# Kernel tuning notes

Hardware: AMD Instinct MI355X
Metric: run time of the kernel (lower is better)

The kernel has to match this reference:

```python
import jax, jax.numpy as jnp
import numpy as np

N_NODES = 100000
N_EDGES = 1600000
EMB = 64
H1 = 128
H2 = 64


def gcn_conv(x, edge_index, W, b, num_nodes):
    # PyG GCNConv: x' = D^{-1/2}(A+I)D^{-1/2} (x W) + b, with self-loops
    x = x @ W  # [N, out]
    src, dst = edge_index[0], edge_index[1]
    loop = jnp.arange(num_nodes, dtype=src.dtype)
    src_f = jnp.concatenate([src, loop])
    dst_f = jnp.concatenate([dst, loop])
    deg = jax.ops.segment_sum(jnp.ones_like(src_f, dtype=x.dtype), dst_f,
                              num_segments=num_nodes)
    dinv = jnp.where(deg > 0, jax.lax.rsqrt(deg), 0.0)
    norm = dinv[src_f] * dinv[dst_f]           # [E+N]
    msg = x[src_f] * norm[:, None]             # gather + scale
    out = jax.ops.segment_sum(msg, dst_f, num_segments=num_nodes)
    return out + b


def setup_inputs() -> dict:
    key = jax.random.key(0)
    ks = jax.random.split(key, 12)
    category_ids = jax.random.randint(ks[0], (N_NODES,), 0, 1000)
    sub_category_ids = jax.random.randint(ks[1], (N_NODES,), 0, 5000)
    element_ids = jax.random.randint(ks[2], (N_NODES,), 0, 100000)
    edge_index = jax.random.randint(ks[3], (2, N_EDGES), 0, N_NODES)
    cat_table = jax.random.normal(ks[4], (1000, EMB), dtype=jnp.float32)
    sub_table = jax.random.normal(ks[5], (5000, EMB), dtype=jnp.float32)
    elem_table = jax.random.normal(ks[6], (100000, EMB), dtype=jnp.float32)
    W1 = jax.random.normal(ks[7], (3 * EMB, H1), dtype=jnp.float32) * (1.0 / np.sqrt(3 * EMB))
    b1 = jnp.zeros((H1,), dtype=jnp.float32)
    W2 = jax.random.normal(ks[8], (H1, H2), dtype=jnp.float32) * (1.0 / np.sqrt(H1))
    b2 = jnp.zeros((H2,), dtype=jnp.float32)
    return {
        "category_ids": category_ids,
        "sub_category_ids": sub_category_ids,
        "element_ids": element_ids,
        "edge_index": edge_index,
        "cat_table": cat_table,
        "sub_table": sub_table,
        "elem_table": elem_table,
        "W1": W1, "b1": b1, "W2": W2, "b2": b2,
    }


def reference(category_ids, sub_category_ids, element_ids, edge_index,
              cat_table, sub_table, elem_table, W1, b1, W2, b2):
    # NodeEmbedding: concat of three 64-dim lookups -> [N, 192]
    x = jnp.concatenate([cat_table[category_ids],
                         sub_table[sub_category_ids],
                         elem_table[element_ids]], axis=-1)
    x = jax.nn.relu(gcn_conv(x, edge_index, W1, b1, N_NODES))
    # dropout(0.3) is identity in eval mode
    x = jax.nn.relu(gcn_conv(x, edge_index, W2, b2, N_NODES))
    return x
```

## Files before the change

### kernel.cpp

```cpp
#include <hip/hip_runtime.h>

#define N_NODES 100000
#define EMB     64
#define H1      128
#define H2      64

#define BSHIFT  7
#define NBUCK   782
#define CAP     3072

#define OFF_DINV  0
#define OFF_ROWP  100004
#define OFF_COL   200008
#define OFF_GFILL 1800008
#define OFF_GBASE 1800792
#define OFF_SCR   1801576
#define OFF_H     4203880
#define OFF_Y     10603880
#define OFF_PCAT  17003880
#define OFF_PSUB  17131880

static __device__ __forceinline__ unsigned short f2bf(float f) {
    unsigned int u = __float_as_uint(f);
    unsigned int r = (u + 0x7fffu + ((u >> 16) & 1u)) >> 16;
    return (unsigned short)r;
}
static __device__ __forceinline__ unsigned int pack2bf(float a, float b) {
    return (unsigned int)f2bf(a) | ((unsigned int)f2bf(b) << 16);
}
static __device__ __forceinline__ float bflo(unsigned int u) {
    return __uint_as_float(u << 16);
}
static __device__ __forceinline__ float bfhi(unsigned int u) {
    return __uint_as_float(u & 0xffff0000u);
}


__global__ __launch_bounds__(1024) void k_bin(
    const int* __restrict__ src, const int* __restrict__ dst, int E,
    int* __restrict__ gfill, unsigned int* __restrict__ scr)
{
    __shared__ int hist[NBUCK];
    __shared__ int basec[NBUCK];
    int t = threadIdx.x;
    for (int i = t; i < NBUCK; i += 1024) hist[i] = 0;
    __syncthreads();
    int chunk = (E + gridDim.x - 1) / gridDim.x;
    int e0 = blockIdx.x * chunk;
    int e1 = min(e0 + chunk, E);
    for (int i = e0 + t; i < e1; i += 1024)
        atomicAdd(&hist[dst[i] >> BSHIFT], 1);
    __syncthreads();
    for (int b = t; b < NBUCK; b += 1024) {
        int c = hist[b];
        basec[b] = (c > 0) ? atomicAdd(&gfill[b], c) : 0;
        hist[b] = 0;
    }
    __syncthreads();
    for (int i = e0 + t; i < e1; i += 1024) {
        int d = dst[i];
        int b = d >> BSHIFT;
        int slot = basec[b] + atomicAdd(&hist[b], 1);
        if (slot < CAP)
            scr[(size_t)b * CAP + slot] =
                ((unsigned int)(d & 127) << 17) | (unsigned int)src[i];
    }
}


__global__ __launch_bounds__(256) void k_bscan(
    const int* __restrict__ gfill, int* __restrict__ gbase,
    int* __restrict__ rowp, int E)
{
    __shared__ int sh[256];
    int t = threadIdx.x;
    int v[4]; int s = 0;
    #pragma unroll
    for (int u = 0; u < 4; ++u) {
        int i = t * 4 + u;
        v[u] = (i < NBUCK) ? gfill[i] : 0;
        s += v[u];
    }
    sh[t] = s;
    __syncthreads();
    for (int off = 1; off < 256; off <<= 1) {
        int x = (t >= off) ? sh[t - off] : 0;
        __syncthreads();
        sh[t] += x;
        __syncthreads();
    }
    int run = (t == 0) ? 0 : sh[t - 1];
    #pragma unroll
    for (int u = 0; u < 4; ++u) {
        int i = t * 4 + u;
        if (i < NBUCK) gbase[i] = run;
        run += v[u];
    }
    if (t == 255) { gbase[NBUCK] = run; rowp[N_NODES] = E; }
}


__global__ __launch_bounds__(512) void k_csr(
    const unsigned int* __restrict__ scr, const int* __restrict__ gfill,
    const int* __restrict__ gbase, int N,
    int* __restrict__ rowp, int* __restrict__ col, float* __restrict__ dinv)
{
    __shared__ unsigned int stage[CAP];
    __shared__ int hist[128];
    __shared__ int offs[128];
    __shared__ int cur[128];
    int b = blockIdx.x, t = threadIdx.x;
    int cnt = gfill[b];
    if (cnt > CAP) cnt = CAP;
    int base = gbase[b];
    if (t < 128) hist[t] = 0;
    __syncthreads();
    for (int i = t; i < cnt; i += 512) {
        unsigned int p = scr[(size_t)b * CAP + i];
        stage[i] = p;
        atomicAdd(&hist[p >> 17], 1);
    }
    __syncthreads();
    if (t < 128) offs[t] = hist[t];
    __syncthreads();
    for (int off = 1; off < 128; off <<= 1) {
        int x = 0;
        if (t < 128 && t >= off) x = offs[t - off];
        __syncthreads();
        if (t < 128) offs[t] += x;
        __syncthreads();
    }
    if (t < 128) {
        int excl = offs[t] - hist[t];
        cur[t] = 0;
        int d = b * 128 + t;
        if (d < N) {
            rowp[d] = base + excl;
            dinv[d] = rsqrtf((float)(hist[t] + 1));
        }
        offs[t] = excl;
    }
    __syncthreads();
    for (int i = t; i < cnt; i += 512) {
        unsigned int p = stage[i];
        int dl = (int)(p >> 17);
        int pos = offs[dl] + atomicAdd(&cur[dl], 1);
        col[base + pos] = (int)(p & 0x1FFFFu);
    }
}


__global__ __launch_bounds__(256) void k_ptab(
    const float* __restrict__ tab, const float* __restrict__ Wseg,
    float* __restrict__ P, int R)
{
    __shared__ float Wl[64][128];
    int t = threadIdx.x;
    for (int idx = t; idx < 64 * 128; idx += 256)
        Wl[idx >> 7][idx & 127] = Wseg[idx];
    __syncthreads();
    int cg = t & 31, ng = t >> 5;
    int r = blockIdx.x * 8 + ng;
    if (r >= R) return;
    const float* x = tab + (size_t)r * 64;
    float4 acc = make_float4(0.f, 0.f, 0.f, 0.f);
    #pragma unroll 8
    for (int k = 0; k < 64; ++k) {
        float xx = x[k];
        float4 w = *(const float4*)&Wl[k][cg * 4];
        acc.x += xx * w.x; acc.y += xx * w.y;
        acc.z += xx * w.z; acc.w += xx * w.w;
    }
    *(float4*)&P[(size_t)r * 128 + cg * 4] = acc;
}


__global__ __launch_bounds__(256) void k_gemm1(
    const int* __restrict__ cid, const int* __restrict__ sid, const int* __restrict__ eid,
    const float* __restrict__ elem_t, const float* __restrict__ W1,
    const float* __restrict__ Pcat, const float* __restrict__ Psub,
    const float* __restrict__ dinv,
    unsigned short* __restrict__ hb, int N)
{
    __shared__ float Wl[64][128];
    int t = threadIdx.x;
    const float* Wc = W1 + 128 * 128;
    for (int idx = t; idx < 64 * 128; idx += 256)
        Wl[idx >> 7][idx & 127] = Wc[idx];
    __syncthreads();

    int cg = t & 31;
    int ng = t >> 5;
    int n0 = blockIdx.x << 6;

    const float* rp[8];
    #pragma unroll
    for (int i = 0; i < 8; ++i) {
        int n = n0 + ng + 8 * i;
        int id = eid[(n < N) ? n : 0];
        rp[i] = elem_t + (size_t)id * 64;
    }
    float4 acc[8];
    #pragma unroll
    for (int i = 0; i < 8; ++i) acc[i] = make_float4(0.f, 0.f, 0.f, 0.f);

    #pragma unroll 4
    for (int k4 = 0; k4 < 16; ++k4) {
        float4 xv[8];
        #pragma unroll
        for (int i = 0; i < 8; ++i)
            xv[i] = *(const float4*)(rp[i] + k4 * 4);
        #pragma unroll
        for (int kk = 0; kk < 4; ++kk) {
            float4 w = *(const float4*)&Wl[k4 * 4 + kk][cg * 4];
            #pragma unroll
            for (int i = 0; i < 8; ++i) {
                float xx = (kk == 0) ? xv[i].x : (kk == 1) ? xv[i].y
                         : (kk == 2) ? xv[i].z : xv[i].w;
                acc[i].x += xx * w.x;
                acc[i].y += xx * w.y;
                acc[i].z += xx * w.z;
                acc[i].w += xx * w.w;
            }
        }
    }
    #pragma unroll
    for (int i = 0; i < 8; ++i) {
        int n = n0 + ng + 8 * i;
        if (n < N) {
            float4 pc = *(const float4*)&Pcat[(size_t)cid[n] * 128 + cg * 4];
            float4 ps = *(const float4*)&Psub[(size_t)sid[n] * 128 + cg * 4];
            float s = dinv[n];
            uint2 p;
            p.x = pack2bf((acc[i].x + pc.x + ps.x) * s, (acc[i].y + pc.y + ps.y) * s);
            p.y = pack2bf((acc[i].z + pc.z + ps.z) * s, (acc[i].w + pc.w + ps.w) * s);
            *(uint2*)(hb + (size_t)n * 128 + cg * 4) = p;
        }
    }
}


__global__ __launch_bounds__(256) void k_gemm2(
    const unsigned int* __restrict__ yb, const float* __restrict__ W2,
    const float* __restrict__ dinv,
    unsigned short* __restrict__ h2b, int N)
{
    __shared__ float Wl[128][64];
    int t = threadIdx.x;
    for (int idx = t; idx < 128 * 64; idx += 256)
        Wl[idx >> 6][idx & 63] = W2[idx];
    __syncthreads();

    int cg = t & 15;
    int ng = t >> 4;
    int n0 = blockIdx.x << 7;
    const unsigned int* rp[8];
    float4 acc[8];
    #pragma unroll
    for (int i = 0; i < 8; ++i) {
        acc[i] = make_float4(0.f, 0.f, 0.f, 0.f);
        int n = n0 + ng + 16 * i;
        rp[i] = yb + (size_t)((n < N) ? n : (N - 1)) * 64;
    }
    #pragma unroll 4
    for (int k4 = 0; k4 < 32; ++k4) {
        uint2 xv[8];
        #pragma unroll
        for (int i = 0; i < 8; ++i)
            xv[i] = *(const uint2*)(rp[i] + k4 * 2);
        #pragma unroll
        for (int kk = 0; kk < 4; ++kk) {
            float4 w = *(const float4*)&Wl[k4 * 4 + kk][cg * 4];
            #pragma unroll
            for (int i = 0; i < 8; ++i) {
                float xx = (kk == 0) ? bflo(xv[i].x) : (kk == 1) ? bfhi(xv[i].x)
                         : (kk == 2) ? bflo(xv[i].y) : bfhi(xv[i].y);
                acc[i].x += xx * w.x;
                acc[i].y += xx * w.y;
                acc[i].z += xx * w.z;
                acc[i].w += xx * w.w;
            }
        }
    }
    #pragma unroll
    for (int i = 0; i < 8; ++i) {
        int n = n0 + ng + 16 * i;
        if (n < N) {
            float s = dinv[n];
            uint2 p;
            p.x = pack2bf(acc[i].x * s, acc[i].y * s);
            p.y = pack2bf(acc[i].z * s, acc[i].w * s);
            *(uint2*)(h2b + (size_t)n * 64 + cg * 4) = p;
        }
    }
}


__global__ __launch_bounds__(256) void k_agg1(
    const unsigned short* __restrict__ hb, const int* __restrict__ rowp,
    const int* __restrict__ col, const float* __restrict__ dinv,
    const float* __restrict__ b1, unsigned int* __restrict__ yb, int N)
{
    int wv = threadIdx.x >> 6;
    int lane = threadIdx.x & 63;
    int d = blockIdx.x * 4 + wv;
    if (d >= N) return;
    const unsigned int* hp = (const unsigned int*)hb;
    float dd = dinv[d];
    unsigned int su = hp[(size_t)d * 64 + lane];
    float ax0 = bflo(su), ay0 = bfhi(su);
    float ax1 = 0.f, ay1 = 0.f, ax2 = 0.f, ay2 = 0.f, ax3 = 0.f, ay3 = 0.f;
    float ax4 = 0.f, ay4 = 0.f, ax5 = 0.f, ay5 = 0.f, ax6 = 0.f, ay6 = 0.f;
    float ax7 = 0.f, ay7 = 0.f;
    int e0 = rowp[d];
    int len = rowp[d + 1] - e0;
    for (int i = 0; i < len; i += 8) {
        int c[8];
        #pragma unroll
        for (int k = 0; k < 8; ++k)
            c[k] = col[(i + k) < len ? (e0 + i + k) : e0];
        #pragma unroll
        for (int k = 0; k < 8; ++k) {
            bool pr = (i + k) < len;
            int idx = pr ? c[k] : d;
            float m = pr ? 1.f : 0.f;
            unsigned int u = hp[(size_t)idx * 64 + lane];
            float vx = m * bflo(u), vy = m * bfhi(u);
            switch (k) {
                case 0: ax0 += vx; ay0 += vy; break;
                case 1: ax1 += vx; ay1 += vy; break;
                case 2: ax2 += vx; ay2 += vy; break;
                case 3: ax3 += vx; ay3 += vy; break;
                case 4: ax4 += vx; ay4 += vy; break;
                case 5: ax5 += vx; ay5 += vy; break;
                case 6: ax6 += vx; ay6 += vy; break;
                default: ax7 += vx; ay7 += vy; break;
            }
        }
    }
    float2 bb = *(const float2*)&b1[lane * 2];
    float rx = dd * (((ax0 + ax1) + (ax2 + ax3)) + ((ax4 + ax5) + (ax6 + ax7))) + bb.x;
    float ry = dd * (((ay0 + ay1) + (ay2 + ay3)) + ((ay4 + ay5) + (ay6 + ay7))) + bb.y;
    yb[(size_t)d * 64 + lane] = pack2bf(rx > 0.f ? rx : 0.f, ry > 0.f ? ry : 0.f);
}


__global__ __launch_bounds__(256) void k_agg2(
    const unsigned short* __restrict__ h2b, const int* __restrict__ rowp,
    const int* __restrict__ col, const float* __restrict__ dinv,
    const float* __restrict__ b2, float* __restrict__ out, int N)
{
    int wv = threadIdx.x >> 6;
    int lane = threadIdx.x & 63;
    int d = blockIdx.x * 4 + wv;
    if (d >= N) return;
    float dd = dinv[d];
    float a0 = __uint_as_float((unsigned int)h2b[(size_t)d * 64 + lane] << 16);
    float a1 = 0.f, a2 = 0.f, a3 = 0.f, a4 = 0.f, a5 = 0.f, a6 = 0.f, a7 = 0.f;
    int e0 = rowp[d];
    int len = rowp[d + 1] - e0;
    for (int i = 0; i < len; i += 8) {
        int c[8];
        #pragma unroll
        for (int k = 0; k < 8; ++k)
            c[k] = col[(i + k) < len ? (e0 + i + k) : e0];
        #pragma unroll
        for (int k = 0; k < 8; ++k) {
            bool pr = (i + k) < len;
            int idx = pr ? c[k] : d;
            float m = pr ? 1.f : 0.f;
            float v = m * __uint_as_float((unsigned int)h2b[(size_t)idx * 64 + lane] << 16);
            switch (k) {
                case 0: a0 += v; break;
                case 1: a1 += v; break;
                case 2: a2 += v; break;
                case 3: a3 += v; break;
                case 4: a4 += v; break;
                case 5: a5 += v; break;
                case 6: a6 += v; break;
                default: a7 += v; break;
            }
        }
    }
    float v = dd * (((a0 + a1) + (a2 + a3)) + ((a4 + a5) + (a6 + a7))) + b2[lane];
    out[(size_t)d * 64 + lane] = v > 0.f ? v : 0.f;
}


extern "C" void kernel_launch(void* const* d_in, const int* in_sizes, int n_in,
                              void* d_out, int out_size, void* d_ws, size_t ws_size,
                              hipStream_t stream) {
    const int*   cid    = (const int*)d_in[0];
    const int*   sid    = (const int*)d_in[1];
    const int*   eid    = (const int*)d_in[2];
    const int*   edge   = (const int*)d_in[3];
    const float* cat_t  = (const float*)d_in[4];
    const float* sub_t  = (const float*)d_in[5];
    const float* elem_t = (const float*)d_in[6];
    const float* W1     = (const float*)d_in[7];
    const float* b1     = (const float*)d_in[8];
    const float* W2     = (const float*)d_in[9];
    const float* b2     = (const float*)d_in[10];
    float* out = (float*)d_out;

    int N = in_sizes[0];
    int E = in_sizes[3] / 2;
    const int* src = edge;
    const int* dst = edge + E;

    int*   ws    = (int*)d_ws;
    float* dinv  = (float*)(ws + OFF_DINV);
    int*   rowp  = ws + OFF_ROWP;
    int*   col   = ws + OFF_COL;
    int*   gfill = ws + OFF_GFILL;
    int*   gbase = ws + OFF_GBASE;
    unsigned int* scr = (unsigned int*)(ws + OFF_SCR);
    unsigned short* hb = (unsigned short*)(ws + OFF_H);
    unsigned int*   yb = (unsigned int*)(ws + OFF_Y);
    float* Pcat = (float*)(ws + OFF_PCAT);
    float* Psub = (float*)(ws + OFF_PSUB);

    hipMemsetAsync(gfill, 0, NBUCK * sizeof(int), stream);

    k_ptab<<<125, 256, 0, stream>>>(cat_t, W1,            Pcat, 1000);
    k_ptab<<<625, 256, 0, stream>>>(sub_t, W1 + 64 * 128, Psub, 5000);

    k_bin<<<200, 1024, 0, stream>>>(src, dst, E, gfill, scr);
    k_bscan<<<1, 256, 0, stream>>>(gfill, gbase, rowp, E);
    k_csr<<<NBUCK, 512, 0, stream>>>(scr, gfill, gbase, N, rowp, col, dinv);

    k_gemm1<<<(N + 63) / 64, 256, 0, stream>>>(cid, sid, eid, elem_t, W1, Pcat, Psub, dinv, hb, N);
    k_agg1<<<(N + 3) / 4, 256, 0, stream>>>(hb, rowp, col, dinv, b1, yb, N);
    k_gemm2<<<(N + 127) / 128, 256, 0, stream>>>(yb, W2, dinv, hb, N);
    k_agg2<<<(N + 3) / 4, 256, 0, stream>>>(hb, rowp, col, dinv, b2, out, N);
}
```

Baseline: 391.0 us.

## Process two destination nodes per wavefront with wider vector gathers in aggregation

Both aggregation kernels now assign two destination nodes to each 64-lane wavefront, one per 32-lane half. Each lane gathers wider vectors: uint2 (4 bf16) in agg1, and in agg2 a 32-bit pair of bf16 instead of a single 16-bit value. The aim is fewer, wider memory transactions per neighbour row and half as many wavefronts. The trade-off is divergence: both halves loop to the larger of the two degrees, with masked loads for the shorter row.

Result: no change. 386.3 us (-1.2%).

```diff
diff --git a/kernel.cpp b/kernel.cpp
--- a/kernel.cpp
+++ b/kernel.cpp
@@ -301,47 +301,55 @@
     const int* __restrict__ col, const float* __restrict__ dinv,
     const float* __restrict__ b1, unsigned int* __restrict__ yb, int N)
 {
-    int wv = threadIdx.x >> 6;
+    int w = blockIdx.x * 4 + (threadIdx.x >> 6);
     int lane = threadIdx.x & 63;
-    int d = blockIdx.x * 4 + wv;
-    if (d >= N) return;
+    int half = lane >> 5, l5 = lane & 31;
+    int d0 = w * 2;
+    if (d0 >= N) return;
+    int d = d0 + half;
+    if (d >= N) d = N - 1;
     const unsigned int* hp = (const unsigned int*)hb;
     float dd = dinv[d];
-    unsigned int su = hp[(size_t)d * 64 + lane];
-    float ax0 = bflo(su), ay0 = bfhi(su);
-    float ax1 = 0.f, ay1 = 0.f, ax2 = 0.f, ay2 = 0.f, ax3 = 0.f, ay3 = 0.f;
-    float ax4 = 0.f, ay4 = 0.f, ax5 = 0.f, ay5 = 0.f, ax6 = 0.f, ay6 = 0.f;
-    float ax7 = 0.f, ay7 = 0.f;
-    int e0 = rowp[d];
-    int len = rowp[d + 1] - e0;
-    for (int i = 0; i < len; i += 8) {
-        int c[8];
-        #pragma unroll
-        for (int k = 0; k < 8; ++k)
-            c[k] = col[(i + k) < len ? (e0 + i + k) : e0];
-        #pragma unroll
-        for (int k = 0; k < 8; ++k) {
+    unsigned base = ((unsigned)d << 6) + (l5 << 1);
+    uint2 su = *(const uint2*)(hp + base);
+    float s00 = bflo(su.x), s01 = bfhi(su.x), s02 = bflo(su.y), s03 = bfhi(su.y);
+    float s10 = 0.f, s11 = 0.f, s12 = 0.f, s13 = 0.f;
+    float s20 = 0.f, s21 = 0.f, s22 = 0.f, s23 = 0.f;
+    float s30 = 0.f, s31 = 0.f, s32 = 0.f, s33 = 0.f;
+    int eb = rowp[d];
+    int len = rowp[d + 1] - eb;
+    int lo = __shfl_xor(len, 32);
+    int lm = len > lo ? len : lo;
+    for (int i = 0; i < lm; i += 4) {
+        int cc[4];
+        #pragma unroll
+        for (int k = 0; k < 4; ++k)
+            cc[k] = col[(i + k) < len ? (eb + i + k) : 0];
+        #pragma unroll
+        for (int k = 0; k < 4; ++k) {
             bool pr = (i + k) < len;
-            int idx = pr ? c[k] : d;
+            int idx = pr ? cc[k] : d;
             float m = pr ? 1.f : 0.f;
-            unsigned int u = hp[(size_t)idx * 64 + lane];
-            float vx = m * bflo(u), vy = m * bfhi(u);
+            uint2 u = *(const uint2*)(hp + (((unsigned)idx) << 6) + (l5 << 1));
+            float vx = m * bflo(u.x), vy = m * bfhi(u.x);
+            float vz = m * bflo(u.y), vw = m * bfhi(u.y);
             switch (k) {
-                case 0: ax0 += vx; ay0 += vy; break;
-                case 1: ax1 += vx; ay1 += vy; break;
-                case 2: ax2 += vx; ay2 += vy; break;
-                case 3: ax3 += vx; ay3 += vy; break;
-                case 4: ax4 += vx; ay4 += vy; break;
-                case 5: ax5 += vx; ay5 += vy; break;
-                case 6: ax6 += vx; ay6 += vy; break;
-                default: ax7 += vx; ay7 += vy; break;
+                case 0: s00 += vx; s01 += vy; s02 += vz; s03 += vw; break;
+                case 1: s10 += vx; s11 += vy; s12 += vz; s13 += vw; break;
+                case 2: s20 += vx; s21 += vy; s22 += vz; s23 += vw; break;
+                default: s30 += vx; s31 += vy; s32 += vz; s33 += vw; break;
             }
         }
     }
-    float2 bb = *(const float2*)&b1[lane * 2];
-    float rx = dd * (((ax0 + ax1) + (ax2 + ax3)) + ((ax4 + ax5) + (ax6 + ax7))) + bb.x;
-    float ry = dd * (((ay0 + ay1) + (ay2 + ay3)) + ((ay4 + ay5) + (ay6 + ay7))) + bb.y;
-    yb[(size_t)d * 64 + lane] = pack2bf(rx > 0.f ? rx : 0.f, ry > 0.f ? ry : 0.f);
+    float4 bb = *(const float4*)&b1[l5 * 4];
+    float r0 = dd * ((s00 + s10) + (s20 + s30)) + bb.x;
+    float r1 = dd * ((s01 + s11) + (s21 + s31)) + bb.y;
+    float r2 = dd * ((s02 + s12) + (s22 + s32)) + bb.z;
+    float r3 = dd * ((s03 + s13) + (s23 + s33)) + bb.w;
+    uint2 p;
+    p.x = pack2bf(r0 > 0.f ? r0 : 0.f, r1 > 0.f ? r1 : 0.f);
+    p.y = pack2bf(r2 > 0.f ? r2 : 0.f, r3 > 0.f ? r3 : 0.f);
+    *(uint2*)(yb + base) = p;
 }
 
 
@@ -350,40 +358,56 @@
     const int* __restrict__ col, const float* __restrict__ dinv,
     const float* __restrict__ b2, float* __restrict__ out, int N)
 {
-    int wv = threadIdx.x >> 6;
+    int w = blockIdx.x * 4 + (threadIdx.x >> 6);
     int lane = threadIdx.x & 63;
-    int d = blockIdx.x * 4 + wv;
-    if (d >= N) return;
+    int half = lane >> 5, l5 = lane & 31;
+    int d0 = w * 2;
+    if (d0 >= N) return;
+    int d = d0 + half;
+    if (d >= N) d = N - 1;
+    const unsigned int* hp = (const unsigned int*)h2b;
     float dd = dinv[d];
-    float a0 = __uint_as_float((unsigned int)h2b[(size_t)d * 64 + lane] << 16);
-    float a1 = 0.f, a2 = 0.f, a3 = 0.f, a4 = 0.f, a5 = 0.f, a6 = 0.f, a7 = 0.f;
-    int e0 = rowp[d];
-    int len = rowp[d + 1] - e0;
-    for (int i = 0; i < len; i += 8) {
-        int c[8];
+    unsigned base = ((unsigned)d << 5) + l5;
+    unsigned su = hp[base];
+    float s00 = bflo(su), s01 = bfhi(su);
+    float s10 = 0.f, s11 = 0.f, s20 = 0.f, s21 = 0.f, s30 = 0.f, s31 = 0.f;
+    float s40 = 0.f, s41 = 0.f, s50 = 0.f, s51 = 0.f, s60 = 0.f, s61 = 0.f;
+    float s70 = 0.f, s71 = 0.f;
+    int eb = rowp[d];
+    int len = rowp[d + 1] - eb;
+    int lo = __shfl_xor(len, 32);
+    int lm = len > lo ? len : lo;
+    for (int i = 0; i < lm; i += 8) {
+        int cc[8];
         #pragma unroll
         for (int k = 0; k < 8; ++k)
-            c[k] = col[(i + k) < len ? (e0 + i + k) : e0];
+            cc[k] = col[(i + k) < len ? (eb + i + k) : 0];
         #pragma unroll
         for (int k = 0; k < 8; ++k) {
             bool pr = (i + k) < len;
-            int idx = pr ? c[k] : d;
+            int idx = pr ? cc[k] : d;
             float m = pr ? 1.f : 0.f;
-            float v = m * __uint_as_float((unsigned int)h2b[(size_t)idx * 64 + lane] << 16);
+            unsigned u = hp[(((unsigned)idx) << 5) + l5];
+            float vx = m * bflo(u), vy = m * bfhi(u);
             switch (k) {
-                case 0: a0 += v; break;
-                case 1: a1 += v; break;
-                case 2: a2 += v; break;
-                case 3: a3 += v; break;
-                case 4: a4 += v; break;
-                case 5: a5 += v; break;
-                case 6: a6 += v; break;
-                default: a7 += v; break;
+                case 0: s00 += vx; s01 += vy; break;
+                case 1: s10 += vx; s11 += vy; break;
+                case 2: s20 += vx; s21 += vy; break;
+                case 3: s30 += vx; s31 += vy; break;
+                case 4: s40 += vx; s41 += vy; break;
+                case 5: s50 += vx; s51 += vy; break;
+                case 6: s60 += vx; s61 += vy; break;
+                default: s70 += vx; s71 += vy; break;
             }
         }
     }
-    float v = dd * (((a0 + a1) + (a2 + a3)) + ((a4 + a5) + (a6 + a7))) + b2[lane];
-    out[(size_t)d * 64 + lane] = v > 0.f ? v : 0.f;
+    float2 bb = *(const float2*)&b2[l5 * 2];
+    float v0 = dd * (((s00 + s10) + (s20 + s30)) + ((s40 + s50) + (s60 + s70))) + bb.x;
+    float v1 = dd * (((s01 + s11) + (s21 + s31)) + ((s41 + s51) + (s61 + s71))) + bb.y;
+    float2 r;
+    r.x = v0 > 0.f ? v0 : 0.f;
+    r.y = v1 > 0.f ? v1 : 0.f;
+    *(float2*)&out[((size_t)d << 6) + (l5 << 1)] = r;
 }
 
 
@@ -430,7 +454,8 @@
     k_csr<<<NBUCK, 512, 0, stream>>>(scr, gfill, gbase, N, rowp, col, dinv);
 
     k_gemm1<<<(N + 63) / 64, 256, 0, stream>>>(cid, sid, eid, elem_t, W1, Pcat, Psub, dinv, hb, N);
-    k_agg1<<<(N + 3) / 4, 256, 0, stream>>>(hb, rowp, col, dinv, b1, yb, N);
+    int aggblk = (N + 7) / 8;
+    k_agg1<<<aggblk, 256, 0, stream>>>(hb, rowp, col, dinv, b1, yb, N);
     k_gemm2<<<(N + 127) / 128, 256, 0, stream>>>(yb, W2, dinv, hb, N);
-    k_agg2<<<(N + 3) / 4, 256, 0, stream>>>(hb, rowp, col, dinv, b2, out, N);
-}
+    k_agg2<<<aggblk, 256, 0, stream>>>(hb, rowp, col, dinv, b2, out, N);
+}
```
